# Kernel tuning notes

Measured on AMD Instinct MI355X. Metric: run time of the kernel, lower is better.

The kernel has to match this reference:

```python
import jax, jax.numpy as jnp
import numpy as np
from jax import lax

B, L, D, F, K = 16, 1024, 384, 1536, 3
MAX_DUR = 10          # clamp on per-token duration (makes output length static)
T_OUT = L * MAX_DUR   # padded expanded length
ALPHA = 1.0
EPS = 1e-5


def conv1d_same(x_ncl, w, b):
    # x_ncl: [B, Cin, L], w: [Cout, Cin, K]
    y = lax.conv_general_dilated(x_ncl, w, window_strides=(1,), padding='SAME',
                                 dimension_numbers=('NCH', 'OIH', 'NCH'))
    return y + b[None, :, None]


def conv_block(x, wA, bA, wB, bB):
    # x: [B, L, D] -> Conv(D->F) ReLU Conv(F->D) ReLU -> [B, L, D]
    h = x.transpose(0, 2, 1)
    h = jax.nn.relu(conv1d_same(h, wA, bA))
    h = jax.nn.relu(conv1d_same(h, wB, bB))
    return h.transpose(0, 2, 1)


def layernorm(x, g, b):
    mu = jnp.mean(x, axis=-1, keepdims=True)
    var = jnp.var(x, axis=-1, keepdims=True)
    return (x - mu) * lax.rsqrt(var + EPS) * g + b


def setup_inputs() -> dict:
    key = jax.random.key(0)
    ks = jax.random.split(key, 8)
    s = 0.02
    return {
        'y': jax.random.normal(ks[0], (B, L, D), jnp.float32),
        'token_lengths': jax.random.randint(ks[1], (B,), 1, L + 1).astype(jnp.int32),
        'w1a': jax.random.normal(ks[2], (F, D, K), jnp.float32) * s,
        'b1a': jnp.zeros((F,), jnp.float32),
        'w1b': jax.random.normal(ks[3], (D, F, K), jnp.float32) * s,
        'b1b': jnp.zeros((D,), jnp.float32),
        'g1': jnp.ones((D,), jnp.float32),
        'be1': jnp.zeros((D,), jnp.float32),
        'w2a': jax.random.normal(ks[4], (F, D, K), jnp.float32) * s,
        'b2a': jnp.zeros((F,), jnp.float32),
        'w2b': jax.random.normal(ks[5], (D, F, K), jnp.float32) * s,
        'b2b': jnp.zeros((D,), jnp.float32),
        'g2': jnp.ones((D,), jnp.float32),
        'be2': jnp.zeros((D,), jnp.float32),
        'wl': jax.random.normal(ks[6], (D, 1), jnp.float32) * s,
        'bl': jnp.zeros((1,), jnp.float32),
    }


def reference(y, token_lengths, w1a, b1a, w1b, b1b, g1, be1,
              w2a, b2a, w2b, b2b, g2, be2, wl, bl):
    # DurationPredictor (eval mode: dropout is identity)
    h = conv_block(y, w1a, b1a, w1b, b1b)
    h = layernorm(h, g1, be1)
    h = conv_block(h, w2a, b2a, w2b, b2b)
    h = layernorm(h, g2, be2)
    preds = h @ wl + bl                      # [B, L, 1]

    # lengths = round(alpha * exp(preds)), masked to valid tokens, clamped
    lns = jnp.round(ALPHA * jnp.exp(preds[..., 0]))
    lns = jnp.clip(lns, 0, MAX_DUR).astype(jnp.int32)        # [B, L]
    mask = jnp.arange(L)[None, :] < token_lengths[:, None]
    lns = jnp.where(mask, lns, 0)

    # ragged repeat_interleave + pad, fully vectorized:
    # output frame t maps to token idx = searchsorted(cumsum(lns), t, 'right')
    csum = jnp.cumsum(lns, axis=1)                            # [B, L]
    totals = csum[:, -1]                                      # [B]
    t = jnp.arange(T_OUT, dtype=jnp.int32)
    idx = jax.vmap(lambda c: jnp.searchsorted(c, t, side='right'))(csum)  # [B, T_OUT]
    idx = jnp.minimum(idx, L - 1)
    gathered = jnp.take_along_axis(y, idx[..., None], axis=1)  # [B, T_OUT, D]
    valid = t[None, :] < totals[:, None]
    enlarged = jnp.where(valid[..., None], gathered, 0.0)
    return enlarged, totals
```

## Files before the change

kernel.cpp:

```cpp
#include <hip/hip_runtime.h>
#include <hip/hip_bf16.h>

#define BB 16
#define LL 1024
#define DD 384
#define FF 1536
#define KK 3
#define T_OUT 10240
#define MAX_DUR 10

#define PADL 1026
#define LO_SCALE 2048.0f
#define LO_INV   4.8828125e-4f

typedef _Float16 f16x8 __attribute__((ext_vector_type(8)));
typedef float    f32x4 __attribute__((ext_vector_type(4)));

__device__ __forceinline__ void gll16(const void* g, void* l) {
    __builtin_amdgcn_global_load_lds(
        (const __attribute__((address_space(1))) void*)g,
        (__attribute__((address_space(3))) void*)l, 16, 0, 0);
}

__device__ __forceinline__ void split_write(float v, _Float16* hi, _Float16* lo, size_t off) {
    _Float16 h = (_Float16)v;
    hi[off] = h;
    lo[off] = (_Float16)((v - (float)h) * LO_SCALE);
}

__device__ __forceinline__ float split_read(const _Float16* hi, const _Float16* lo, size_t off) {
    return (float)hi[off] + (float)lo[off] * LO_INV;
}

__global__ void wsplit_k(const float* __restrict__ w, _Float16* __restrict__ hi,
                         _Float16* __restrict__ lo, int O, int I) {
    int id = blockIdx.x * 256 + threadIdx.x;
    int n = O * I * 3;
    if (id >= n) return;
    int o = id / (3 * I);
    int rem = id - o * 3 * I;
    int k = rem / I;
    int i = rem - k * I;
    float v = w[(o * I + i) * 3 + k];
    split_write(v, hi, lo, id);
}

__global__ void ysplit_k(const float* __restrict__ y, _Float16* __restrict__ hi,
                         _Float16* __restrict__ lo) {
    int id = blockIdx.x * 256 + threadIdx.x;
    if (id >= BB * PADL * DD) return;
    int d = id % DD;
    int r = id / DD;
    int b = r / PADL;
    int lr = r - b * PADL;
    float v = 0.f;
    if (lr >= 1 && lr <= LL) v = y[((size_t)(b << 10) + (lr - 1)) * DD + d];
    split_write(v, hi, lo, id);
}

__global__ void padzero_k(_Float16* __restrict__ hi, _Float16* __restrict__ lo, int width) {
    int id = blockIdx.x * 256 + threadIdx.x;
    if (id >= BB * 2 * width) return;
    int b = id / (2 * width);
    int rem = id - b * 2 * width;
    int row = (rem / width) ? (PADL - 1) : 0;
    int c = rem % width;
    size_t off = (size_t)(b * PADL + row) * width + c;
    hi[off] = (_Float16)0.f;
    lo[off] = (_Float16)0.f;
}

__global__ __launch_bounds__(256, 2) void gemm_split(
        const _Float16* __restrict__ Ahi, const _Float16* __restrict__ Alo,
        const _Float16* __restrict__ Whi, const _Float16* __restrict__ Wlo,
        const float* __restrict__ bias,
        _Float16* __restrict__ Ohi, _Float16* __restrict__ Olo,
        int Cin, int Cout, int Ktot, int nN) {
    __shared__ _Float16 lds_h[32768];
    const int tid = threadIdx.x;
    const int lane = tid & 63;
    const int w = tid >> 6;
    const int lm = lane & 15, lq = lane >> 4;
    const int j = blockIdx.x;
    const int xcd = j & 7;
    const int t2 = j >> 3;
    const int n_t = t2 % nN;
    const int mt = (t2 / nN) * 8 + xcd;
    const int m0 = mt << 7;
    const int n0 = n_t << 7;
    const int b = m0 >> 10;
    const int l0 = m0 & 1023;
    const int rowBase = b * PADL + l0;
    const int wm = (w >> 1) * 64, wn = (w & 1) * 64;

    f32x4 accM[4][4], accC[4][4];
    const f32x4 zz = {0.f, 0.f, 0.f, 0.f};
    #pragma unroll
    for (int i = 0; i < 4; ++i)
        #pragma unroll
        for (int jj = 0; jj < 4; ++jj) { accM[i][jj] = zz; accC[i][jj] = zz; }

    const int nKT = Ktot >> 5;

    auto stage = [&](int kt, int nxt) {
        int kseg = kt % 3;
        int d0 = (kt / 3) << 5;
        int kk0 = kseg * Cin + d0;
        #pragma unroll
        for (int it = 0; it < 2; ++it) {
            int s = (w * 2 + it) * 64 + lane;
            int p = s >> 3, sl = s & 7;
            int t = sl ^ (p & 7);
            int m = p * 2 + (t >> 2);
            int k8 = t & 3;
            size_t aoff = (size_t)(rowBase + m + kseg) * Cin + d0 + k8 * 8;
            size_t boff = (size_t)(n0 + m) * Ktot + kk0 + k8 * 8;
            _Float16* lbase = lds_h + nxt * 16384 + (size_t)(w * 2 + it) * 512;
            gll16(Ahi + aoff, lbase);
            gll16(Alo + aoff, lbase + 4096);
            gll16(Whi + boff, lbase + 8192);
            gll16(Wlo + boff, lbase + 12288);
        }
    };

    stage(0, 0);
    for (int kt = 0; kt < nKT; ++kt) {
        const int cur = kt & 1;
        __syncthreads();
        if (kt + 1 < nKT) stage(kt + 1, cur ^ 1);
        const _Float16* lb = lds_h + cur * 16384;
        f16x8 aH[4], aL[4], bH[4], bL[4];
        #pragma unroll
        for (int i = 0; i < 4; ++i) {
            int m = wm + i * 16 + lm;
            int p = m >> 1;
            int sl = (((m & 1) << 2) | lq) ^ (p & 7);
            int off = p * 64 + sl * 8;
            aH[i] = *(const f16x8*)(lb + off);
            aL[i] = *(const f16x8*)(lb + 4096 + off);
            int n = wn + i * 16 + lm;
            int pn = n >> 1;
            int sln = (((n & 1) << 2) | lq) ^ (pn & 7);
            int offn = pn * 64 + sln * 8;
            bH[i] = *(const f16x8*)(lb + 8192 + offn);
            bL[i] = *(const f16x8*)(lb + 12288 + offn);
        }
        #pragma unroll
        for (int i = 0; i < 4; ++i)
            #pragma unroll
            for (int jj = 0; jj < 4; ++jj) {
                accM[i][jj] = __builtin_amdgcn_mfma_f32_16x16x32_f16(aH[i], bH[jj], accM[i][jj], 0, 0, 0);
                accC[i][jj] = __builtin_amdgcn_mfma_f32_16x16x32_f16(aH[i], bL[jj], accC[i][jj], 0, 0, 0);
                accC[i][jj] = __builtin_amdgcn_mfma_f32_16x16x32_f16(aL[i], bH[jj], accC[i][jj], 0, 0, 0);
            }
    }
    #pragma unroll
    for (int i = 0; i < 4; ++i)
        #pragma unroll
        for (int jj = 0; jj < 4; ++jj) {
            int n_g = n0 + wn + jj * 16 + lm;
            float bv = bias[n_g];
            #pragma unroll
            for (int r = 0; r < 4; ++r) {
                int l = l0 + wm + i * 16 + lq * 4 + r;
                float v = accM[i][jj][r] + accC[i][jj][r] * LO_INV + bv;
                v = fmaxf(v, 0.f);
                size_t off = (size_t)(b * PADL + 1 + l) * Cout + n_g;
                split_write(v, Ohi, Olo, off);
            }
        }
}

__global__ __launch_bounds__(128) void ln_split_k(
        _Float16* __restrict__ hi, _Float16* __restrict__ lo,
        const float* __restrict__ g, const float* __restrict__ be) {
    const int row = blockIdx.x;
    const int b = row >> 10, l = row & 1023;
    const size_t base = (size_t)(b * PADL + 1 + l) * DD;
    const int tid = threadIdx.x;
    float v0 = split_read(hi, lo, base + tid);
    float v1 = split_read(hi, lo, base + tid + 128);
    float v2 = split_read(hi, lo, base + tid + 256);

    __shared__ float sh[2];
    float s = v0 + v1 + v2;
    #pragma unroll
    for (int o = 32; o > 0; o >>= 1) s += __shfl_down(s, o, 64);
    if ((tid & 63) == 0) sh[tid >> 6] = s;
    __syncthreads();
    float mu = (sh[0] + sh[1]) * (1.f / DD);
    __syncthreads();
    float d0 = v0 - mu, d1 = v1 - mu, d2 = v2 - mu;
    float q = d0 * d0 + d1 * d1 + d2 * d2;
    #pragma unroll
    for (int o = 32; o > 0; o >>= 1) q += __shfl_down(q, o, 64);
    if ((tid & 63) == 0) sh[tid >> 6] = q;
    __syncthreads();
    float var = (sh[0] + sh[1]) * (1.f / DD);
    float rs = rsqrtf(var + 1e-5f);
    split_write(d0 * rs * g[tid] + be[tid], hi, lo, base + tid);
    split_write(d1 * rs * g[tid + 128] + be[tid + 128], hi, lo, base + tid + 128);
    split_write(d2 * rs * g[tid + 256] + be[tid + 256], hi, lo, base + tid + 256);
}

__global__ __launch_bounds__(128) void ln_pred_split_k(
        const _Float16* __restrict__ hi, const _Float16* __restrict__ lo,
        const float* __restrict__ g, const float* __restrict__ be,
        const float* __restrict__ wl, const float* __restrict__ bl,
        const int* __restrict__ token_lengths, int* __restrict__ lns) {
    const int row = blockIdx.x;
    const int b = row >> 10, l = row & 1023;
    const size_t base = (size_t)(b * PADL + 1 + l) * DD;
    const int tid = threadIdx.x;
    float v0 = split_read(hi, lo, base + tid);
    float v1 = split_read(hi, lo, base + tid + 128);
    float v2 = split_read(hi, lo, base + tid + 256);

    __shared__ float sh[2];
    float s = v0 + v1 + v2;
    #pragma unroll
    for (int o = 32; o > 0; o >>= 1) s += __shfl_down(s, o, 64);
    if ((tid & 63) == 0) sh[tid >> 6] = s;
    __syncthreads();
    float mu = (sh[0] + sh[1]) * (1.f / DD);
    __syncthreads();
    float d0 = v0 - mu, d1 = v1 - mu, d2 = v2 - mu;
    float q = d0 * d0 + d1 * d1 + d2 * d2;
    #pragma unroll
    for (int o = 32; o > 0; o >>= 1) q += __shfl_down(q, o, 64);
    if ((tid & 63) == 0) sh[tid >> 6] = q;
    __syncthreads();
    float var = (sh[0] + sh[1]) * (1.f / DD);
    float rs = rsqrtf(var + 1e-5f);
    __syncthreads();
    float p = (d0 * rs * g[tid]       + be[tid])       * wl[tid]
            + (d1 * rs * g[tid + 128] + be[tid + 128]) * wl[tid + 128]
            + (d2 * rs * g[tid + 256] + be[tid + 256]) * wl[tid + 256];
    #pragma unroll
    for (int o = 32; o > 0; o >>= 1) p += __shfl_down(p, o, 64);
    if ((tid & 63) == 0) sh[tid >> 6] = p;
    __syncthreads();
    if (tid == 0) {
        float pred = sh[0] + sh[1] + bl[0];
        float e = expf(pred);
        float r = rintf(e);
        r = fminf(fmaxf(r, 0.f), (float)MAX_DUR);
        int v = (int)r;
        if (l >= token_lengths[b]) v = 0;
        lns[row] = v;
    }
}

__global__ __launch_bounds__(1024) void cumsum_k(
        const int* __restrict__ lns, int* __restrict__ csum,
        float* __restrict__ totals_out) {
    __shared__ int s[1024];
    const int b = blockIdx.x, tid = threadIdx.x;
    s[tid] = lns[(b << 10) + tid];
    __syncthreads();
    #pragma unroll
    for (int o = 1; o < 1024; o <<= 1) {
        int t = (tid >= o) ? s[tid - o] : 0;
        __syncthreads();
        s[tid] += t;
        __syncthreads();
    }
    csum[(b << 10) + tid] = s[tid];
    if (tid == 1023) totals_out[b] = (float)s[1023];
}

__global__ __launch_bounds__(256) void gather_k(
        const float* __restrict__ y, const int* __restrict__ csum,
        float* __restrict__ out) {
    int gid = blockIdx.x * 256 + threadIdx.x;
    int c4 = gid % 96;
    int rest = gid / 96;
    int t = rest % T_OUT;
    int b = rest / T_OUT;
    const int* c = csum + (b << 10);
    int total = c[1023];
    float4 r = make_float4(0.f, 0.f, 0.f, 0.f);
    if (t < total) {
        int lo = 0, hi = 1024;
        while (lo < hi) {
            int mid = (lo + hi) >> 1;
            if (c[mid] <= t) lo = mid + 1; else hi = mid;
        }
        int idx = min(lo, LL - 1);
        r = *(const float4*)(y + ((size_t)((b << 10) + idx)) * DD + (c4 << 2));
    }
    *(float4*)(out + ((size_t)b * T_OUT + t) * DD + (c4 << 2)) = r;
}

extern "C" void kernel_launch(void* const* d_in, const int* in_sizes, int n_in,
                              void* d_out, int out_size, void* d_ws, size_t ws_size,
                              hipStream_t stream) {
    const float* y   = (const float*)d_in[0];
    const int*   tok = (const int*)d_in[1];
    const float* w1a = (const float*)d_in[2];
    const float* b1a = (const float*)d_in[3];
    const float* w1b = (const float*)d_in[4];
    const float* b1b = (const float*)d_in[5];
    const float* g1  = (const float*)d_in[6];
    const float* be1 = (const float*)d_in[7];
    const float* w2a = (const float*)d_in[8];
    const float* b2a = (const float*)d_in[9];
    const float* w2b = (const float*)d_in[10];
    const float* b2b = (const float*)d_in[11];
    const float* g2  = (const float*)d_in[12];
    const float* be2 = (const float*)d_in[13];
    const float* wl  = (const float*)d_in[14];
    const float* bl  = (const float*)d_in[15];

    float* out = (float*)d_out;

    const size_t WN   = (size_t)FF * DD * KK;
    const size_t SN   = (size_t)BB * PADL * DD;
    const size_t H1N  = (size_t)BB * PADL * FF;
    _Float16* p = (_Float16*)d_ws;
    _Float16* Wh1a = p;              _Float16* Wl1a = Wh1a + WN;
    _Float16* Wh1b = Wl1a + WN;      _Float16* Wl1b = Wh1b + WN;
    _Float16* Wh2a = Wl1b + WN;      _Float16* Wl2a = Wh2a + WN;
    _Float16* Wh2b = Wl2a + WN;      _Float16* Wl2b = Wh2b + WN;
    _Float16* Shi  = Wl2b + WN;      _Float16* Slo  = Shi + SN;
    _Float16* H1hi = Slo + SN;       _Float16* H1lo = H1hi + H1N;
    int* lns  = (int*)(H1lo + H1N);
    int* csum = lns + BB * LL;

    const int M = BB * LL;

    {
        int n = FF * DD * KK;
        wsplit_k<<<(n + 255) / 256, 256, 0, stream>>>(w1a, Wh1a, Wl1a, FF, DD);
        wsplit_k<<<(n + 255) / 256, 256, 0, stream>>>(w1b, Wh1b, Wl1b, DD, FF);
        wsplit_k<<<(n + 255) / 256, 256, 0, stream>>>(w2a, Wh2a, Wl2a, FF, DD);
        wsplit_k<<<(n + 255) / 256, 256, 0, stream>>>(w2b, Wh2b, Wl2b, DD, FF);
        int ny = BB * PADL * DD;
        ysplit_k<<<(ny + 255) / 256, 256, 0, stream>>>(y, Shi, Slo);
        int np = BB * 2 * FF;
        padzero_k<<<(np + 255) / 256, 256, 0, stream>>>(H1hi, H1lo, FF);
    }
    gemm_split<<<(FF / 128) * (M / 128), 256, 0, stream>>>(Shi, Slo, Wh1a, Wl1a, b1a, H1hi, H1lo, DD, FF, 3 * DD, FF / 128);
    gemm_split<<<(DD / 128) * (M / 128), 256, 0, stream>>>(H1hi, H1lo, Wh1b, Wl1b, b1b, Shi, Slo, FF, DD, 3 * FF, DD / 128);
    ln_split_k<<<M, 128, 0, stream>>>(Shi, Slo, g1, be1);
    gemm_split<<<(FF / 128) * (M / 128), 256, 0, stream>>>(Shi, Slo, Wh2a, Wl2a, b2a, H1hi, H1lo, DD, FF, 3 * DD, FF / 128);
    gemm_split<<<(DD / 128) * (M / 128), 256, 0, stream>>>(H1hi, H1lo, Wh2b, Wl2b, b2b, Shi, Slo, FF, DD, 3 * FF, DD / 128);
    ln_pred_split_k<<<M, 128, 0, stream>>>(Shi, Slo, g2, be2, wl, bl, tok, lns);
    cumsum_k<<<BB, 1024, 0, stream>>>(lns, csum, out + (size_t)BB * T_OUT * DD);
    {
        long long n = (long long)BB * T_OUT * 96;
        gather_k<<<(int)((n + 255) / 256), 256, 0, stream>>>(y, csum, out);
    }
}
```

Baseline: 1.036 ms.

## Pre-swizzle weights into MFMA fragment layout and load B directly from global

Weights are reordered at split time into per-lane MFMA fragment order, so the GEMM loads B operands straight from global/L2 into registers instead of staging them through LDS. This halves LDS use per block and removes the B LDS writes and reads. The block-to-tile mapping is also changed to group four M tiles per N tile, which should improve L2 reuse of weights. The cost is global-load latency on B inside the k-loop, with no double buffering for those loads.

New measurement: 1.035 ms. About the same (-0.1%).

```diff
diff --git a/kernel.cpp b/kernel.cpp
--- a/kernel.cpp
+++ b/kernel.cpp
@@ -32,16 +32,22 @@
     return (float)hi[off] + (float)lo[off] * LO_INV;
 }
 
-__global__ void wsplit_k(const float* __restrict__ w, _Float16* __restrict__ hi,
-                         _Float16* __restrict__ lo, int O, int I) {
+__global__ void wfrag_k(const float* __restrict__ w, _Float16* __restrict__ hi,
+                        _Float16* __restrict__ lo, int O, int I) {
     int id = blockIdx.x * 256 + threadIdx.x;
-    int n = O * I * 3;
-    if (id >= n) return;
-    int o = id / (3 * I);
-    int rem = id - o * 3 * I;
-    int k = rem / I;
-    int i = rem - k * I;
-    float v = w[(o * I + i) * 3 + k];
+    int total = O * 3 * I;
+    if (id >= total) return;
+    int e = id & 7;
+    int lane = (id >> 3) & 63;
+    int rest = id >> 9;
+    int nKT = (3 * I) >> 5;
+    int ktl = rest % nKT;
+    int ot = rest / nKT;
+    int o = ot * 16 + (lane & 15);
+    int koff = ((lane >> 4) << 3) + e;
+    int kseg = ktl % 3;
+    int i = (ktl / 3) * 32 + koff;
+    float v = w[(o * I + i) * 3 + kseg];
     split_write(v, hi, lo, id);
 }
 
@@ -72,21 +78,23 @@
 
 __global__ __launch_bounds__(256, 2) void gemm_split(
         const _Float16* __restrict__ Ahi, const _Float16* __restrict__ Alo,
-        const _Float16* __restrict__ Whi, const _Float16* __restrict__ Wlo,
+        const _Float16* __restrict__ WfH, const _Float16* __restrict__ WfL,
         const float* __restrict__ bias,
         _Float16* __restrict__ Ohi, _Float16* __restrict__ Olo,
         int Cin, int Cout, int Ktot, int nN) {
-    __shared__ _Float16 lds_h[32768];
+    __shared__ _Float16 lds_h[16384];
     const int tid = threadIdx.x;
     const int lane = tid & 63;
     const int w = tid >> 6;
     const int lm = lane & 15, lq = lane >> 4;
-    const int j = blockIdx.x;
-    const int xcd = j & 7;
-    const int t2 = j >> 3;
-    const int n_t = t2 % nN;
-    const int mt = (t2 / nN) * 8 + xcd;
-    const int m0 = mt << 7;
+    const int xcd = blockIdx.x & 7;
+    const int t2 = blockIdx.x >> 3;
+    const int g  = t2 / (4 * nN);
+    const int r  = t2 - g * (4 * nN);
+    const int n_t = r >> 2;
+    const int mi  = r & 3;
+    const int m_t = ((g * 4 + mi) << 3) + xcd;
+    const int m0 = m_t << 7;
     const int n0 = n_t << 7;
     const int b = m0 >> 10;
     const int l0 = m0 & 1023;
@@ -102,10 +110,9 @@
 
     const int nKT = Ktot >> 5;
 
-    auto stage = [&](int kt, int nxt) {
+    auto stageA = [&](int kt, int nxt) {
         int kseg = kt % 3;
         int d0 = (kt / 3) << 5;
-        int kk0 = kseg * Cin + d0;
         #pragma unroll
         for (int it = 0; it < 2; ++it) {
             int s = (w * 2 + it) * 64 + lane;
@@ -114,22 +121,27 @@
             int m = p * 2 + (t >> 2);
             int k8 = t & 3;
             size_t aoff = (size_t)(rowBase + m + kseg) * Cin + d0 + k8 * 8;
-            size_t boff = (size_t)(n0 + m) * Ktot + kk0 + k8 * 8;
-            _Float16* lbase = lds_h + nxt * 16384 + (size_t)(w * 2 + it) * 512;
+            _Float16* lbase = lds_h + nxt * 8192 + (size_t)(w * 2 + it) * 512;
             gll16(Ahi + aoff, lbase);
             gll16(Alo + aoff, lbase + 4096);
-            gll16(Whi + boff, lbase + 8192);
-            gll16(Wlo + boff, lbase + 12288);
         }
     };
 
-    stage(0, 0);
+    stageA(0, 0);
     for (int kt = 0; kt < nKT; ++kt) {
         const int cur = kt & 1;
         __syncthreads();
-        if (kt + 1 < nKT) stage(kt + 1, cur ^ 1);
-        const _Float16* lb = lds_h + cur * 16384;
-        f16x8 aH[4], aL[4], bH[4], bL[4];
+        f16x8 bH[4], bL[4];
+        #pragma unroll
+        for (int jj = 0; jj < 4; ++jj) {
+            int ntg = (n0 + wn + jj * 16) >> 4;
+            size_t boff = (((size_t)ntg * nKT + kt) * 64 + lane) * 8;
+            bH[jj] = *(const f16x8*)(WfH + boff);
+            bL[jj] = *(const f16x8*)(WfL + boff);
+        }
+        if (kt + 1 < nKT) stageA(kt + 1, cur ^ 1);
+        const _Float16* lb = lds_h + cur * 8192;
+        f16x8 aH[4], aL[4];
         #pragma unroll
         for (int i = 0; i < 4; ++i) {
             int m = wm + i * 16 + lm;
@@ -138,17 +150,11 @@
             int off = p * 64 + sl * 8;
             aH[i] = *(const f16x8*)(lb + off);
             aL[i] = *(const f16x8*)(lb + 4096 + off);
-            int n = wn + i * 16 + lm;
-            int pn = n >> 1;
-            int sln = (((n & 1) << 2) | lq) ^ (pn & 7);
-            int offn = pn * 64 + sln * 8;
-            bH[i] = *(const f16x8*)(lb + 8192 + offn);
-            bL[i] = *(const f16x8*)(lb + 12288 + offn);
-        }
-        #pragma unroll
-        for (int i = 0; i < 4; ++i)
+        }
+        #pragma unroll
+        for (int jj = 0; jj < 4; ++jj)
             #pragma unroll
-            for (int jj = 0; jj < 4; ++jj) {
+            for (int i = 0; i < 4; ++i) {
                 accM[i][jj] = __builtin_amdgcn_mfma_f32_16x16x32_f16(aH[i], bH[jj], accM[i][jj], 0, 0, 0);
                 accC[i][jj] = __builtin_amdgcn_mfma_f32_16x16x32_f16(aH[i], bL[jj], accC[i][jj], 0, 0, 0);
                 accC[i][jj] = __builtin_amdgcn_mfma_f32_16x16x32_f16(aL[i], bH[jj], accC[i][jj], 0, 0, 0);
@@ -161,9 +167,9 @@
             int n_g = n0 + wn + jj * 16 + lm;
             float bv = bias[n_g];
             #pragma unroll
-            for (int r = 0; r < 4; ++r) {
-                int l = l0 + wm + i * 16 + lq * 4 + r;
-                float v = accM[i][jj][r] + accC[i][jj][r] * LO_INV + bv;
+            for (int rr = 0; rr < 4; ++rr) {
+                int l = l0 + wm + i * 16 + lq * 4 + rr;
+                float v = accM[i][jj][rr] + accC[i][jj][rr] * LO_INV + bv;
                 v = fmaxf(v, 0.f);
                 size_t off = (size_t)(b * PADL + 1 + l) * Cout + n_g;
                 split_write(v, Ohi, Olo, off);
@@ -331,10 +337,10 @@
 
     {
         int n = FF * DD * KK;
-        wsplit_k<<<(n + 255) / 256, 256, 0, stream>>>(w1a, Wh1a, Wl1a, FF, DD);
-        wsplit_k<<<(n + 255) / 256, 256, 0, stream>>>(w1b, Wh1b, Wl1b, DD, FF);
-        wsplit_k<<<(n + 255) / 256, 256, 0, stream>>>(w2a, Wh2a, Wl2a, FF, DD);
-        wsplit_k<<<(n + 255) / 256, 256, 0, stream>>>(w2b, Wh2b, Wl2b, DD, FF);
+        wfrag_k<<<(n + 255) / 256, 256, 0, stream>>>(w1a, Wh1a, Wl1a, FF, DD);
+        wfrag_k<<<(n + 255) / 256, 256, 0, stream>>>(w1b, Wh1b, Wl1b, DD, FF);
+        wfrag_k<<<(n + 255) / 256, 256, 0, stream>>>(w2a, Wh2a, Wl2a, FF, DD);
+        wfrag_k<<<(n + 255) / 256, 256, 0, stream>>>(w2b, Wh2b, Wl2b, DD, FF);
         int ny = BB * PADL * DD;
         ysplit_k<<<(ny + 255) / 256, 256, 0, stream>>>(y, Shi, Slo);
         int np = BB * 2 * FF;
```
